# Kernel optimization log

Measured on AMD Instinct MI355X. Metric: run time of the kernel, lower is better.

Reference implementation:

```python
import jax, jax.numpy as jnp
import numpy as np

NUM_NODES = 94
SEQ_LEN = 784
OUT_CLASSES = 10
ALPHA = 0.5
GAMMA = 0.1
OMEGA = 2.0 * np.pi / 28.0
H = 1.0
INV_SQRT_N = 1.0 / np.sqrt(NUM_NODES)


def _xavier(key, shape):
    fan_in, fan_out = shape[1], shape[0]
    limit = np.sqrt(6.0 / (fan_in + fan_out))
    return jax.random.uniform(key, shape, jnp.float32, -limit, limit)


def setup_inputs() -> dict:
    key = jax.random.key(0)
    k_in, k_ih, k_hh, k_ro = jax.random.split(key, 4)
    batch = 1024
    return {
        "input_sequence": jax.random.normal(k_in, (batch, SEQ_LEN), jnp.float32),
        "w_ih": _xavier(k_ih, (NUM_NODES, 1)),   # Linear(1 -> N) weight
        "b_ih": jnp.zeros((NUM_NODES,), jnp.float32),
        "w_hh": _xavier(k_hh, (NUM_NODES, NUM_NODES)),  # Linear(N -> N) weight
        "b_hh": jnp.zeros((NUM_NODES,), jnp.float32),
        "w_ro": _xavier(k_ro, (OUT_CLASSES, NUM_NODES)),  # readout weight
        "b_ro": jnp.zeros((OUT_CLASSES,), jnp.float32),
    }


def reference(input_sequence, w_ih, b_ih, w_hh, b_hh, w_ro, b_ro):
    batch = input_sequence.shape[0]
    # precompute external drive for all steps: [T, B, N]
    # W_ih(s_t) with input_dim=1 is an outer product: s_t * w_ih[:,0] + b_ih
    s = input_sequence.T  # [T, B]
    w_ih_vec = w_ih[:, 0]  # [N]

    def step(carry, s_t):
        x, y = carry
        I_ext = s_t[:, None] * w_ih_vec[None, :] + b_ih  # [B, N]
        I_rec = y @ w_hh.T + b_hh                        # [B, N]
        A = (I_ext + I_rec) * INV_SQRT_N
        accel = ALPHA * jnp.tanh(A) - 2.0 * GAMMA * y - (OMEGA ** 2) * x
        x_new = x + H * y
        y_new = y + H * accel
        return (x_new, y_new), None

    x0 = jnp.zeros((batch, NUM_NODES), jnp.float32)
    y0 = jnp.zeros((batch, NUM_NODES), jnp.float32)
    (x_final, _), _ = jax.lax.scan(step, (x0, y0), s)
    return x_final @ w_ro.T + b_ro  # [B, 10]
```

## Files before the change

### kernel.cpp

```cpp
#include <hip/hip_runtime.h>
#include <math.h>

#define NUM_NODES 94
#define SEQ_LEN 784
#define OUT_CLASSES 10
#define EPB 16
#define NW 6
#define YP 104
#define SP 796

#define TWO_GAMMA 0.2f
#define OM2 0.0503551324598949f
#define INV_SQRT_N 0.103142124625879
#define LOG2E 1.4426950408889634
#define WSCALE ((float)(2.0 * INV_SQRT_N * LOG2E))

typedef _Float16 half8 __attribute__((ext_vector_type(8)));
typedef _Float16 half4 __attribute__((ext_vector_type(4)));
typedef float    floatx4 __attribute__((ext_vector_type(4)));
typedef float    f2 __attribute__((ext_vector_type(2)));

__global__
__attribute__((amdgpu_flat_work_group_size(NW*64, NW*64)))
void horn_kernel(
    const float* __restrict__ input,
    const float* __restrict__ w_ih,
    const float* __restrict__ b_ih,
    const float* __restrict__ w_hh,
    const float* __restrict__ b_hh,
    const float* __restrict__ w_ro,
    const float* __restrict__ b_ro,
    float* __restrict__ out)
{
    __shared__ __align__(16) float    sinl[EPB * SP];
    __shared__ __align__(16) _Float16 ybuf[2][EPB * YP];

    const int tid  = threadIdx.x;
    const int m    = tid >> 6;
    const int lane = tid & 63;
    const int e    = lane & 15;
    const int h    = lane >> 4;
    const int bb   = blockIdx.x;

    {
        const floatx4* in4 = (const floatx4*)(input + (size_t)bb * EPB * SEQ_LEN);
        for (int idx = tid; idx < EPB * (SEQ_LEN / 4); idx += NW * 64) {
            int ee = idx / (SEQ_LEN / 4);
            int cc = idx - ee * (SEQ_LEN / 4);
            *(floatx4*)&sinl[ee * SP + 4 * cc] = in4[idx];
        }
    }
    {
        float* yz = (float*)&ybuf[0][0];
        for (int i = tid; i < (2 * EPB * YP) / 2; i += NW * 64) yz[i] = 0.0f;
    }

    const int arow = 16 * m + e;
    half8 a0, a1, a2;
    #pragma unroll
    for (int i = 0; i < 8; i++) {
        const int kb = 8 * h + i;
        a0[i] = (_Float16)((arow < NUM_NODES && kb      < NUM_NODES) ? w_hh[arow * NUM_NODES + kb     ] * WSCALE : 0.0f);
        a1[i] = (_Float16)((arow < NUM_NODES && kb + 32 < NUM_NODES) ? w_hh[arow * NUM_NODES + kb + 32] * WSCALE : 0.0f);
        a2[i] = (_Float16)((arow < NUM_NODES && kb + 64 < NUM_NODES) ? w_hh[arow * NUM_NODES + kb + 64] * WSCALE : 0.0f);
    }

    const int r0 = 16 * m + 4 * h;
    f2 wih01, wih23, bias01, bias23;
    {
        float w[4], b[4];
        #pragma unroll
        for (int i = 0; i < 4; i++) {
            const int r = r0 + i;
            w[i] = (r < NUM_NODES) ? w_ih[r] * WSCALE : 0.0f;
            b[i] = (r < NUM_NODES) ? (b_ih[r] + b_hh[r]) * WSCALE : 0.0f;
        }
        wih01[0] = w[0]; wih01[1] = w[1]; wih23[0] = w[2]; wih23[1] = w[3];
        bias01[0] = b[0]; bias01[1] = b[1]; bias23[0] = b[2]; bias23[1] = b[3];
    }

    f2 x01 = {0.0f, 0.0f}, x23 = {0.0f, 0.0f};
    f2 y01 = {0.0f, 0.0f}, y23 = {0.0f, 0.0f};

    const int rdoff = e * YP + 8 * h;
    const int wroff = e * YP + r0;
    const int sbase = e * SP;

    const floatx4 zf4 = {0.0f, 0.0f, 0.0f, 0.0f};
    const f2 ng = {-TWO_GAMMA, -TWO_GAMMA};
    const f2 no = {-OM2, -OM2};

    __syncthreads();

    #define HSTEP(RD, WR, T) do {                                                  \
        half8 b0 = *(const half8*)&(RD)[rdoff];                                    \
        half8 b1 = *(const half8*)&(RD)[rdoff + 32];                               \
        half8 b2 = *(const half8*)&(RD)[rdoff + 64];                               \
        float st = sinl[sbase + (T)];                                              \
        floatx4 d0 = __builtin_amdgcn_mfma_f32_16x16x32_f16(a0, b0, zf4, 0, 0, 0); \
        floatx4 d1 = __builtin_amdgcn_mfma_f32_16x16x32_f16(a1, b1, zf4, 0, 0, 0); \
        floatx4 d2 = __builtin_amdgcn_mfma_f32_16x16x32_f16(a2, b2, zf4, 0, 0, 0); \
        f2 S01 = { d0[0] + d1[0] + d2[0], d0[1] + d1[1] + d2[1] };                 \
        f2 S23 = { d0[2] + d1[2] + d2[2], d0[3] + d1[3] + d2[3] };                 \
        f2 st2 = { st, st };                                                       \
        f2 e01 = st2 * wih01 + (bias01 + S01);                                     \
        f2 e23 = st2 * wih23 + (bias23 + S23);                                     \
        f2 t01, t23;                                                               \
        t01[0] = 0.5f - __builtin_amdgcn_rcpf(__builtin_amdgcn_exp2f(e01[0]) + 1.0f); \
        t01[1] = 0.5f - __builtin_amdgcn_rcpf(__builtin_amdgcn_exp2f(e01[1]) + 1.0f); \
        t23[0] = 0.5f - __builtin_amdgcn_rcpf(__builtin_amdgcn_exp2f(e23[0]) + 1.0f); \
        t23[1] = 0.5f - __builtin_amdgcn_rcpf(__builtin_amdgcn_exp2f(e23[1]) + 1.0f); \
        t01 = ng * y01 + t01;  t01 = no * x01 + t01;                               \
        t23 = ng * y23 + t23;  t23 = no * x23 + t23;                               \
        x01 += y01;  x23 += y23;                                                   \
        y01 += t01;  y23 += t23;                                                   \
        half4 yh;                                                                  \
        yh[0] = (_Float16)y01[0]; yh[1] = (_Float16)y01[1];                        \
        yh[2] = (_Float16)y23[0]; yh[3] = (_Float16)y23[1];                        \
        *(half4*)&(WR)[wroff] = yh;                                                \
        __syncthreads();                                                           \
    } while (0)

    for (int t = 0; t < SEQ_LEN; t += 2) {
        HSTEP(ybuf[0], ybuf[1], t);
        HSTEP(ybuf[1], ybuf[0], t + 1);
    }
    #undef HSTEP

    float* xsh = sinl;
    {
        floatx4 xv = { x01[0], x01[1], x23[0], x23[1] };
        *(floatx4*)&xsh[e * YP + r0] = xv;
    }
    __syncthreads();

    if (tid < EPB * OUT_CLASSES) {
        const int ee = tid / OUT_CLASSES;
        const int c  = tid - ee * OUT_CLASSES;
        float acc = b_ro[c];
        #pragma unroll 2
        for (int r = 0; r < NUM_NODES; r++)
            acc += xsh[ee * YP + r] * w_ro[c * NUM_NODES + r];
        out[((size_t)bb * EPB + ee) * OUT_CLASSES + c] = acc;
    }
}

extern "C" void kernel_launch(void* const* d_in, const int* in_sizes, int n_in,
                              void* d_out, int out_size, void* d_ws, size_t ws_size,
                              hipStream_t stream) {
    const float* input = (const float*)d_in[0];
    const float* w_ih  = (const float*)d_in[1];
    const float* b_ih  = (const float*)d_in[2];
    const float* w_hh  = (const float*)d_in[3];
    const float* b_hh  = (const float*)d_in[4];
    const float* w_ro  = (const float*)d_in[5];
    const float* b_ro  = (const float*)d_in[6];
    float* out = (float*)d_out;

    const int batch = in_sizes[0] / SEQ_LEN;
    dim3 grid(batch / EPB);
    dim3 block(NW * 64);

    hipLaunchKernelGGL(horn_kernel, grid, block, 0, stream,
                       input, w_ih, b_ih, w_hh, b_hh, w_ro, b_ro, out);
}
```

Before: 293.3 us.

## Process 32 batch elements per block with 4 waves each owning 48 rows

Doubles the batch elements per block to 32 and reorganizes work into 4 waves. Each wave handles 16 elements and 48 of the hidden rows, issuing 9 chained MFMAs per step with the bias folded into the accumulator. Because the larger element count no longer fits in LDS, input is staged in two halves of the sequence. The aim is fewer blocks and cheaper barriers among 4 waves instead of 6, at the cost of more serial MFMA and transcendental work per wave on each recurrent step and half as many blocks occupying CUs.

```diff
diff --git a/kernel.cpp b/kernel.cpp
--- a/kernel.cpp
+++ b/kernel.cpp
@@ -4,10 +4,10 @@
 #define NUM_NODES 94
 #define SEQ_LEN 784
 #define OUT_CLASSES 10
-#define EPB 16
-#define NW 6
+#define EPB 32
 #define YP 104
-#define SP 796
+#define SP 396
+#define THALF 392
 
 #define TWO_GAMMA 0.2f
 #define OM2 0.0503551324598949f
@@ -21,7 +21,7 @@
 typedef float    f2 __attribute__((ext_vector_type(2)));
 
 __global__
-__attribute__((amdgpu_flat_work_group_size(NW*64, NW*64)))
+__attribute__((amdgpu_flat_work_group_size(256, 256)))
 void horn_kernel(
     const float* __restrict__ input,
     const float* __restrict__ w_ih,
@@ -36,110 +36,127 @@
     __shared__ __align__(16) _Float16 ybuf[2][EPB * YP];
 
     const int tid  = threadIdx.x;
-    const int m    = tid >> 6;
+    const int w    = tid >> 6;
     const int lane = tid & 63;
+    const int g    = w >> 1;
+    const int tau  = w & 1;
     const int e    = lane & 15;
     const int h    = lane >> 4;
     const int bb   = blockIdx.x;
+    const int Eloc = 16 * g + e;
+    const int RB   = 48 * tau;
 
-    {
-        const floatx4* in4 = (const floatx4*)(input + (size_t)bb * EPB * SEQ_LEN);
-        for (int idx = tid; idx < EPB * (SEQ_LEN / 4); idx += NW * 64) {
-            int ee = idx / (SEQ_LEN / 4);
-            int cc = idx - ee * (SEQ_LEN / 4);
-            *(floatx4*)&sinl[ee * SP + 4 * cc] = in4[idx];
+    for (int i = tid; i < (2 * EPB * YP) / 2; i += 256) ((float*)ybuf)[i] = 0.0f;
+
+    half8 a[3][3];
+    floatx4 biasC[3];
+    f2 wih01[3], wih23[3];
+    #pragma unroll
+    for (int t3 = 0; t3 < 3; ++t3) {
+        const int arow = RB + 16 * t3 + e;
+        #pragma unroll
+        for (int c = 0; c < 3; ++c) {
+            #pragma unroll
+            for (int i = 0; i < 8; ++i) {
+                const int k = 32 * c + 8 * h + i;
+                a[t3][c][i] = (_Float16)((arow < NUM_NODES && k < NUM_NODES)
+                                ? w_hh[arow * NUM_NODES + k] * WSCALE : 0.0f);
+            }
         }
-    }
-    {
-        float* yz = (float*)&ybuf[0][0];
-        for (int i = tid; i < (2 * EPB * YP) / 2; i += NW * 64) yz[i] = 0.0f;
+        float bv[4], wv[4];
+        #pragma unroll
+        for (int r = 0; r < 4; ++r) {
+            const int R = RB + 16 * t3 + 4 * h + r;
+            bv[r] = (R < NUM_NODES) ? (b_ih[R] + b_hh[R]) * WSCALE : 0.0f;
+            wv[r] = (R < NUM_NODES) ? w_ih[R] * WSCALE : 0.0f;
+        }
+        biasC[t3][0] = bv[0]; biasC[t3][1] = bv[1]; biasC[t3][2] = bv[2]; biasC[t3][3] = bv[3];
+        wih01[t3][0] = wv[0]; wih01[t3][1] = wv[1];
+        wih23[t3][0] = wv[2]; wih23[t3][1] = wv[3];
     }
 
-    const int arow = 16 * m + e;
-    half8 a0, a1, a2;
+    f2 x01[3], x23[3], y01[3], y23[3];
     #pragma unroll
-    for (int i = 0; i < 8; i++) {
-        const int kb = 8 * h + i;
-        a0[i] = (_Float16)((arow < NUM_NODES && kb      < NUM_NODES) ? w_hh[arow * NUM_NODES + kb     ] * WSCALE : 0.0f);
-        a1[i] = (_Float16)((arow < NUM_NODES && kb + 32 < NUM_NODES) ? w_hh[arow * NUM_NODES + kb + 32] * WSCALE : 0.0f);
-        a2[i] = (_Float16)((arow < NUM_NODES && kb + 64 < NUM_NODES) ? w_hh[arow * NUM_NODES + kb + 64] * WSCALE : 0.0f);
+    for (int t3 = 0; t3 < 3; ++t3) {
+        x01[t3] = (f2){0.0f, 0.0f}; x23[t3] = (f2){0.0f, 0.0f};
+        y01[t3] = (f2){0.0f, 0.0f}; y23[t3] = (f2){0.0f, 0.0f};
     }
 
-    const int r0 = 16 * m + 4 * h;
-    f2 wih01, wih23, bias01, bias23;
-    {
-        float w[4], b[4];
-        #pragma unroll
-        for (int i = 0; i < 4; i++) {
-            const int r = r0 + i;
-            w[i] = (r < NUM_NODES) ? w_ih[r] * WSCALE : 0.0f;
-            b[i] = (r < NUM_NODES) ? (b_ih[r] + b_hh[r]) * WSCALE : 0.0f;
-        }
-        wih01[0] = w[0]; wih01[1] = w[1]; wih23[0] = w[2]; wih23[1] = w[3];
-        bias01[0] = b[0]; bias01[1] = b[1]; bias23[0] = b[2]; bias23[1] = b[3];
-    }
+    const int rb  = Eloc * YP + 8 * h;
+    const int wb0 = Eloc * YP + RB + 4 * h;
+    const int sb  = Eloc * SP;
 
-    f2 x01 = {0.0f, 0.0f}, x23 = {0.0f, 0.0f};
-    f2 y01 = {0.0f, 0.0f}, y23 = {0.0f, 0.0f};
-
-    const int rdoff = e * YP + 8 * h;
-    const int wroff = e * YP + r0;
-    const int sbase = e * SP;
-
-    const floatx4 zf4 = {0.0f, 0.0f, 0.0f, 0.0f};
     const f2 ng = {-TWO_GAMMA, -TWO_GAMMA};
     const f2 no = {-OM2, -OM2};
 
-    __syncthreads();
-
-    #define HSTEP(RD, WR, T) do {                                                  \
-        half8 b0 = *(const half8*)&(RD)[rdoff];                                    \
-        half8 b1 = *(const half8*)&(RD)[rdoff + 32];                               \
-        half8 b2 = *(const half8*)&(RD)[rdoff + 64];                               \
-        float st = sinl[sbase + (T)];                                              \
-        floatx4 d0 = __builtin_amdgcn_mfma_f32_16x16x32_f16(a0, b0, zf4, 0, 0, 0); \
-        floatx4 d1 = __builtin_amdgcn_mfma_f32_16x16x32_f16(a1, b1, zf4, 0, 0, 0); \
-        floatx4 d2 = __builtin_amdgcn_mfma_f32_16x16x32_f16(a2, b2, zf4, 0, 0, 0); \
-        f2 S01 = { d0[0] + d1[0] + d2[0], d0[1] + d1[1] + d2[1] };                 \
-        f2 S23 = { d0[2] + d1[2] + d2[2], d0[3] + d1[3] + d2[3] };                 \
-        f2 st2 = { st, st };                                                       \
-        f2 e01 = st2 * wih01 + (bias01 + S01);                                     \
-        f2 e23 = st2 * wih23 + (bias23 + S23);                                     \
-        f2 t01, t23;                                                               \
-        t01[0] = 0.5f - __builtin_amdgcn_rcpf(__builtin_amdgcn_exp2f(e01[0]) + 1.0f); \
-        t01[1] = 0.5f - __builtin_amdgcn_rcpf(__builtin_amdgcn_exp2f(e01[1]) + 1.0f); \
-        t23[0] = 0.5f - __builtin_amdgcn_rcpf(__builtin_amdgcn_exp2f(e23[0]) + 1.0f); \
-        t23[1] = 0.5f - __builtin_amdgcn_rcpf(__builtin_amdgcn_exp2f(e23[1]) + 1.0f); \
-        t01 = ng * y01 + t01;  t01 = no * x01 + t01;                               \
-        t23 = ng * y23 + t23;  t23 = no * x23 + t23;                               \
-        x01 += y01;  x23 += y23;                                                   \
-        y01 += t01;  y23 += t23;                                                   \
-        half4 yh;                                                                  \
-        yh[0] = (_Float16)y01[0]; yh[1] = (_Float16)y01[1];                        \
-        yh[2] = (_Float16)y23[0]; yh[3] = (_Float16)y23[1];                        \
-        *(half4*)&(WR)[wroff] = yh;                                                \
-        __syncthreads();                                                           \
+    #define HSTEP(RD, WR, T) do {                                                      \
+        const _Float16* yr = &(RD)[rb];                                                \
+        half8 B0 = *(const half8*)(yr);                                                \
+        half8 B1 = *(const half8*)(yr + 32);                                           \
+        half8 B2 = *(const half8*)(yr + 64);                                           \
+        float st = sinl[sb + (T)];                                                     \
+        f2 st2 = {st, st};                                                             \
+        _Float16* yw = &(WR)[wb0];                                                     \
+        _Pragma("unroll")                                                              \
+        for (int t3 = 0; t3 < 3; ++t3) {                                               \
+            floatx4 d = biasC[t3];                                                     \
+            d = __builtin_amdgcn_mfma_f32_16x16x32_f16(a[t3][0], B0, d, 0, 0, 0);      \
+            d = __builtin_amdgcn_mfma_f32_16x16x32_f16(a[t3][1], B1, d, 0, 0, 0);      \
+            d = __builtin_amdgcn_mfma_f32_16x16x32_f16(a[t3][2], B2, d, 0, 0, 0);      \
+            f2 S01 = {d[0], d[1]}, S23 = {d[2], d[3]};                                 \
+            f2 e01 = st2 * wih01[t3] + S01;                                            \
+            f2 e23 = st2 * wih23[t3] + S23;                                            \
+            f2 t01, t23;                                                               \
+            t01[0] = 0.5f - __builtin_amdgcn_rcpf(__builtin_amdgcn_exp2f(e01[0]) + 1.0f); \
+            t01[1] = 0.5f - __builtin_amdgcn_rcpf(__builtin_amdgcn_exp2f(e01[1]) + 1.0f); \
+            t23[0] = 0.5f - __builtin_amdgcn_rcpf(__builtin_amdgcn_exp2f(e23[0]) + 1.0f); \
+            t23[1] = 0.5f - __builtin_amdgcn_rcpf(__builtin_amdgcn_exp2f(e23[1]) + 1.0f); \
+            t01 = ng * y01[t3] + t01;  t01 = no * x01[t3] + t01;                       \
+            t23 = ng * y23[t3] + t23;  t23 = no * x23[t3] + t23;                       \
+            x01[t3] += y01[t3];  x23[t3] += y23[t3];                                   \
+            y01[t3] += t01;      y23[t3] += t23;                                       \
+            half4 yh;                                                                  \
+            yh[0] = (_Float16)y01[t3][0]; yh[1] = (_Float16)y01[t3][1];                \
+            yh[2] = (_Float16)y23[t3][0]; yh[3] = (_Float16)y23[t3][1];                \
+            *(half4*)(yw + 16 * t3) = yh;                                              \
+        }                                                                              \
+        __syncthreads();                                                               \
     } while (0)
 
-    for (int t = 0; t < SEQ_LEN; t += 2) {
-        HSTEP(ybuf[0], ybuf[1], t);
-        HSTEP(ybuf[1], ybuf[0], t + 1);
+    for (int hf = 0; hf < 2; ++hf) {
+        __syncthreads();
+        {
+            const float* src = input + (size_t)bb * EPB * SEQ_LEN + hf * THALF;
+            for (int idx = tid; idx < EPB * (THALF / 4); idx += 256) {
+                int ee = idx / (THALF / 4);
+                int cc = idx - ee * (THALF / 4);
+                *(floatx4*)&sinl[ee * SP + 4 * cc] =
+                    *(const floatx4*)(src + (size_t)ee * SEQ_LEN + 4 * cc);
+            }
+        }
+        __syncthreads();
+        for (int t = 0; t < THALF; t += 2) {
+            HSTEP(ybuf[0], ybuf[1], t);
+            HSTEP(ybuf[1], ybuf[0], t + 1);
+        }
     }
     #undef HSTEP
 
     float* xsh = sinl;
-    {
-        floatx4 xv = { x01[0], x01[1], x23[0], x23[1] };
-        *(floatx4*)&xsh[e * YP + r0] = xv;
+    #pragma unroll
+    for (int t3 = 0; t3 < 3; ++t3) {
+        floatx4 xv;
+        xv[0] = x01[t3][0]; xv[1] = x01[t3][1]; xv[2] = x23[t3][0]; xv[3] = x23[t3][1];
+        *(floatx4*)&xsh[Eloc * YP + RB + 16 * t3 + 4 * h] = xv;
     }
     __syncthreads();
 
-    if (tid < EPB * OUT_CLASSES) {
-        const int ee = tid / OUT_CLASSES;
-        const int c  = tid - ee * OUT_CLASSES;
+    for (int idx = tid; idx < EPB * OUT_CLASSES; idx += 256) {
+        const int ee = idx / OUT_CLASSES;
+        const int c  = idx - ee * OUT_CLASSES;
         float acc = b_ro[c];
         #pragma unroll 2
-        for (int r = 0; r < NUM_NODES; r++)
+        for (int r = 0; r < NUM_NODES; ++r)
             acc += xsh[ee * YP + r] * w_ro[c * NUM_NODES + r];
         out[((size_t)bb * EPB + ee) * OUT_CLASSES + c] = acc;
     }
@@ -159,7 +176,7 @@
 
     const int batch = in_sizes[0] / SEQ_LEN;
     dim3 grid(batch / EPB);
-    dim3 block(NW * 64);
+    dim3 block(256);
 
     hipLaunchKernelGGL(horn_kernel, grid, block, 0, stream,
                        input, w_ih, b_ih, w_hh, b_hh, w_ro, b_ro, out);
```

Result: slower. 405.0 us (+38.1%).

## Use four waves with uneven row-tile split and MFMA bias accumulation

Applied to the files above, without the earlier changes.

Reduces the workgroup from six waves to four. The first two waves each compute two 16-row tiles of the recurrent matvec and the last two waves compute one each. The bias is folded into the MFMA accumulator init and two of the three MFMAs are chained, which removes some adds. The next step's input sample is prefetched one step ahead to take its shared load off the critical path. Fewer waves means cheaper barriers, but it makes the work per step uneven, so waves 0 and 1 now sit on the per-step critical path with twice the MFMA and tanh work.

```diff
diff --git a/kernel.cpp b/kernel.cpp
--- a/kernel.cpp
+++ b/kernel.cpp
@@ -5,9 +5,9 @@
 #define SEQ_LEN 784
 #define OUT_CLASSES 10
 #define EPB 16
-#define NW 6
+#define NW 4
 #define YP 104
-#define SP 796
+#define SP 788
 
 #define TWO_GAMMA 0.2f
 #define OM2 0.0503551324598949f
@@ -36,88 +36,114 @@
     __shared__ __align__(16) _Float16 ybuf[2][EPB * YP];
 
     const int tid  = threadIdx.x;
-    const int m    = tid >> 6;
+    const int w    = tid >> 6;
     const int lane = tid & 63;
     const int e    = lane & 15;
     const int h    = lane >> 4;
     const int bb   = blockIdx.x;
+
+    const int  TA  = (w < 2) ? 2 * w : (w + 2);
+    const int  TB  = 2 * w + 1;
+    const bool two = (w < 2);
 
     {
         const floatx4* in4 = (const floatx4*)(input + (size_t)bb * EPB * SEQ_LEN);
         for (int idx = tid; idx < EPB * (SEQ_LEN / 4); idx += NW * 64) {
             int ee = idx / (SEQ_LEN / 4);
             int cc = idx - ee * (SEQ_LEN / 4);
-            *(floatx4*)&sinl[ee * SP + 4 * cc] = in4[idx];
+            *(floatx4*)&sinl[ee * SP + 4 * cc] = in4[ee * (SEQ_LEN / 4) + cc];
         }
     }
-    {
-        float* yz = (float*)&ybuf[0][0];
-        for (int i = tid; i < (2 * EPB * YP) / 2; i += NW * 64) yz[i] = 0.0f;
-    }
+    for (int i = tid; i < (2 * EPB * YP) / 2; i += NW * 64) ((float*)ybuf)[i] = 0.0f;
 
-    const int arow = 16 * m + e;
-    half8 a0, a1, a2;
-    #pragma unroll
-    for (int i = 0; i < 8; i++) {
-        const int kb = 8 * h + i;
-        a0[i] = (_Float16)((arow < NUM_NODES && kb      < NUM_NODES) ? w_hh[arow * NUM_NODES + kb     ] * WSCALE : 0.0f);
-        a1[i] = (_Float16)((arow < NUM_NODES && kb + 32 < NUM_NODES) ? w_hh[arow * NUM_NODES + kb + 32] * WSCALE : 0.0f);
-        a2[i] = (_Float16)((arow < NUM_NODES && kb + 64 < NUM_NODES) ? w_hh[arow * NUM_NODES + kb + 64] * WSCALE : 0.0f);
-    }
+    #define LOAD_TILE(T, A0, A1, A2, BIASC, WIH01, WIH23) do {                     \
+        const int arow = 16 * (T) + e;                                             \
+        _Pragma("unroll")                                                          \
+        for (int i = 0; i < 8; ++i) {                                              \
+            const int k = 8 * h + i;                                               \
+            (A0)[i] = (_Float16)((arow < NUM_NODES && k      < NUM_NODES)          \
+                        ? w_hh[arow * NUM_NODES + k     ] * WSCALE : 0.0f);        \
+            (A1)[i] = (_Float16)((arow < NUM_NODES && k + 32 < NUM_NODES)          \
+                        ? w_hh[arow * NUM_NODES + k + 32] * WSCALE : 0.0f);        \
+            (A2)[i] = (_Float16)((arow < NUM_NODES && k + 64 < NUM_NODES)          \
+                        ? w_hh[arow * NUM_NODES + k + 64] * WSCALE : 0.0f);        \
+        }                                                                          \
+        _Pragma("unroll")                                                          \
+        for (int r = 0; r < 4; ++r) {                                              \
+            const int R = 16 * (T) + 4 * h + r;                                    \
+            const float bv = (R < NUM_NODES) ? (b_ih[R] + b_hh[R]) * WSCALE : 0.0f;\
+            const float wv = (R < NUM_NODES) ? w_ih[R] * WSCALE : 0.0f;            \
+            (BIASC)[r] = bv;                                                       \
+            if (r < 2) (WIH01)[r] = wv; else (WIH23)[r - 2] = wv;                   \
+        }                                                                          \
+    } while (0)
 
-    const int r0 = 16 * m + 4 * h;
-    f2 wih01, wih23, bias01, bias23;
-    {
-        float w[4], b[4];
-        #pragma unroll
-        for (int i = 0; i < 4; i++) {
-            const int r = r0 + i;
-            w[i] = (r < NUM_NODES) ? w_ih[r] * WSCALE : 0.0f;
-            b[i] = (r < NUM_NODES) ? (b_ih[r] + b_hh[r]) * WSCALE : 0.0f;
-        }
-        wih01[0] = w[0]; wih01[1] = w[1]; wih23[0] = w[2]; wih23[1] = w[3];
-        bias01[0] = b[0]; bias01[1] = b[1]; bias23[0] = b[2]; bias23[1] = b[3];
-    }
+    half8 aA0, aA1, aA2, aB0, aB1, aB2;
+    floatx4 biasA = {0,0,0,0}, biasB = {0,0,0,0};
+    f2 wihA01 = {0,0}, wihA23 = {0,0}, wihB01 = {0,0}, wihB23 = {0,0};
+    LOAD_TILE(TA, aA0, aA1, aA2, biasA, wihA01, wihA23);
+    if (two) { LOAD_TILE(TB, aB0, aB1, aB2, biasB, wihB01, wihB23); }
+    #undef LOAD_TILE
 
-    f2 x01 = {0.0f, 0.0f}, x23 = {0.0f, 0.0f};
-    f2 y01 = {0.0f, 0.0f}, y23 = {0.0f, 0.0f};
+    f2 xA01 = {0,0}, xA23 = {0,0}, yA01 = {0,0}, yA23 = {0,0};
+    f2 xB01 = {0,0}, xB23 = {0,0}, yB01 = {0,0}, yB23 = {0,0};
 
-    const int rdoff = e * YP + 8 * h;
-    const int wroff = e * YP + r0;
-    const int sbase = e * SP;
+    const int rb  = e * YP + 8 * h;
+    const int wbA = e * YP + 16 * TA + 4 * h;
+    const int wbB = e * YP + 16 * TB + 4 * h;
+    const int sb  = e * SP;
 
-    const floatx4 zf4 = {0.0f, 0.0f, 0.0f, 0.0f};
+    const floatx4 zf4 = {0,0,0,0};
     const f2 ng = {-TWO_GAMMA, -TWO_GAMMA};
     const f2 no = {-OM2, -OM2};
 
     __syncthreads();
 
-    #define HSTEP(RD, WR, T) do {                                                  \
-        half8 b0 = *(const half8*)&(RD)[rdoff];                                    \
-        half8 b1 = *(const half8*)&(RD)[rdoff + 32];                               \
-        half8 b2 = *(const half8*)&(RD)[rdoff + 64];                               \
-        float st = sinl[sbase + (T)];                                              \
-        floatx4 d0 = __builtin_amdgcn_mfma_f32_16x16x32_f16(a0, b0, zf4, 0, 0, 0); \
-        floatx4 d1 = __builtin_amdgcn_mfma_f32_16x16x32_f16(a1, b1, zf4, 0, 0, 0); \
-        floatx4 d2 = __builtin_amdgcn_mfma_f32_16x16x32_f16(a2, b2, zf4, 0, 0, 0); \
-        f2 S01 = { d0[0] + d1[0] + d2[0], d0[1] + d1[1] + d2[1] };                 \
-        f2 S23 = { d0[2] + d1[2] + d2[2], d0[3] + d1[3] + d2[3] };                 \
+    float st = sinl[sb];
+
+    #define DYN(d, WIH01, WIH23, X01, X23, Y01, Y23, WR, WOFF) do {                \
         f2 st2 = { st, st };                                                       \
-        f2 e01 = st2 * wih01 + (bias01 + S01);                                     \
-        f2 e23 = st2 * wih23 + (bias23 + S23);                                     \
+        f2 e01 = st2 * (WIH01) + (f2){ (d)[0], (d)[1] };                           \
+        f2 e23 = st2 * (WIH23) + (f2){ (d)[2], (d)[3] };                           \
         f2 t01, t23;                                                               \
         t01[0] = 0.5f - __builtin_amdgcn_rcpf(__builtin_amdgcn_exp2f(e01[0]) + 1.0f); \
         t01[1] = 0.5f - __builtin_amdgcn_rcpf(__builtin_amdgcn_exp2f(e01[1]) + 1.0f); \
         t23[0] = 0.5f - __builtin_amdgcn_rcpf(__builtin_amdgcn_exp2f(e23[0]) + 1.0f); \
         t23[1] = 0.5f - __builtin_amdgcn_rcpf(__builtin_amdgcn_exp2f(e23[1]) + 1.0f); \
-        t01 = ng * y01 + t01;  t01 = no * x01 + t01;                               \
-        t23 = ng * y23 + t23;  t23 = no * x23 + t23;                               \
-        x01 += y01;  x23 += y23;                                                   \
-        y01 += t01;  y23 += t23;                                                   \
+        t01 = ng * (Y01) + t01;  t01 = no * (X01) + t01;                           \
+        t23 = ng * (Y23) + t23;  t23 = no * (X23) + t23;                           \
+        (X01) += (Y01);  (X23) += (Y23);                                           \
+        (Y01) += t01;    (Y23) += t23;                                             \
         half4 yh;                                                                  \
-        yh[0] = (_Float16)y01[0]; yh[1] = (_Float16)y01[1];                        \
-        yh[2] = (_Float16)y23[0]; yh[3] = (_Float16)y23[1];                        \
-        *(half4*)&(WR)[wroff] = yh;                                                \
+        yh[0] = (_Float16)(Y01)[0]; yh[1] = (_Float16)(Y01)[1];                    \
+        yh[2] = (_Float16)(Y23)[0]; yh[3] = (_Float16)(Y23)[1];                    \
+        *(half4*)&(WR)[WOFF] = yh;                                                 \
+    } while (0)
+
+    #define HSTEP(RD, WR, T) do {                                                  \
+        const _Float16* yr = &(RD)[rb];                                            \
+        half8 B0 = *(const half8*)(yr);                                            \
+        half8 B1 = *(const half8*)(yr + 32);                                       \
+        half8 B2 = *(const half8*)(yr + 64);                                       \
+        const int tn = ((T) + 1 < SEQ_LEN) ? (T) + 1 : (SEQ_LEN - 1);              \
+        float stn = sinl[sb + tn];                                                 \
+                         \
+        floatx4 dA  = __builtin_amdgcn_mfma_f32_16x16x32_f16(aA0, B0, biasA, 0, 0, 0); \
+        floatx4 dA2 = __builtin_amdgcn_mfma_f32_16x16x32_f16(aA1, B1, zf4,  0, 0, 0); \
+        dA = __builtin_amdgcn_mfma_f32_16x16x32_f16(aA2, B2, dA, 0, 0, 0);         \
+        if (two) {                                                                 \
+            floatx4 dB  = __builtin_amdgcn_mfma_f32_16x16x32_f16(aB0, B0, biasB, 0, 0, 0); \
+            floatx4 dB2 = __builtin_amdgcn_mfma_f32_16x16x32_f16(aB1, B1, zf4,  0, 0, 0); \
+            dB = __builtin_amdgcn_mfma_f32_16x16x32_f16(aB2, B2, dB, 0, 0, 0);     \
+            dB += dB2;                                                             \
+            dA += dA2;                                                             \
+            DYN(dA, wihA01, wihA23, xA01, xA23, yA01, yA23, WR, wbA);              \
+            DYN(dB, wihB01, wihB23, xB01, xB23, yB01, yB23, WR, wbB);              \
+        } else {                                                                   \
+            dA += dA2;                                                             \
+            DYN(dA, wihA01, wihA23, xA01, xA23, yA01, yA23, WR, wbA);              \
+        }                                                                          \
+        st = stn;                                                                  \
         __syncthreads();                                                           \
     } while (0)
 
@@ -126,20 +152,27 @@
         HSTEP(ybuf[1], ybuf[0], t + 1);
     }
     #undef HSTEP
+    #undef DYN
 
     float* xsh = sinl;
     {
-        floatx4 xv = { x01[0], x01[1], x23[0], x23[1] };
-        *(floatx4*)&xsh[e * YP + r0] = xv;
+        floatx4 xv;
+        xv[0] = xA01[0]; xv[1] = xA01[1]; xv[2] = xA23[0]; xv[3] = xA23[1];
+        *(floatx4*)&xsh[e * YP + 16 * TA + 4 * h] = xv;
+        if (two) {
+            floatx4 xw;
+            xw[0] = xB01[0]; xw[1] = xB01[1]; xw[2] = xB23[0]; xw[3] = xB23[1];
+            *(floatx4*)&xsh[e * YP + 16 * TB + 4 * h] = xw;
+        }
     }
     __syncthreads();
 
-    if (tid < EPB * OUT_CLASSES) {
-        const int ee = tid / OUT_CLASSES;
-        const int c  = tid - ee * OUT_CLASSES;
+    for (int idx = tid; idx < EPB * OUT_CLASSES; idx += NW * 64) {
+        const int ee = idx / OUT_CLASSES;
+        const int c  = idx - ee * OUT_CLASSES;
         float acc = b_ro[c];
         #pragma unroll 2
-        for (int r = 0; r < NUM_NODES; r++)
+        for (int r = 0; r < NUM_NODES; ++r)
             acc += xsh[ee * YP + r] * w_ro[c * NUM_NODES + r];
         out[((size_t)bb * EPB + ee) * OUT_CLASSES + c] = acc;
     }
```

New measurement: 332.8 us. +13.4%, slower.

## Fold input drive and bias into MFMA via augmented y columns

Applied to the files above, without the earlier changes.

Folds the external drive and bias into the recurrent matrix product. The A matrix gains two extra columns (w_ih and the combined bias), and the y buffer carries the next input sample and a constant 1 in columns 94 and 95, written each step by one duty lane group. The y row stride gets an e-dependent pad to change the LDS bank mapping, and the damping/spring update is regrouped so that only a subtraction follows the tanh. This removes per-lane input loads and FMAs from the critical path, at the cost of rounding the input and bias to fp16, extra divergent branches, and a tail-store special case.

```diff
diff --git a/kernel.cpp b/kernel.cpp
--- a/kernel.cpp
+++ b/kernel.cpp
@@ -6,8 +6,8 @@
 #define OUT_CLASSES 10
 #define EPB 16
 #define NW 6
-#define YP 104
-#define SP 796
+#define SP 788
+#define YHALF 1664
 
 #define TWO_GAMMA 0.2f
 #define OM2 0.0503551324598949f
@@ -17,6 +17,7 @@
 
 typedef _Float16 half8 __attribute__((ext_vector_type(8)));
 typedef _Float16 half4 __attribute__((ext_vector_type(4)));
+typedef _Float16 half2v __attribute__((ext_vector_type(2)));
 typedef float    floatx4 __attribute__((ext_vector_type(4)));
 typedef float    f2 __attribute__((ext_vector_type(2)));
 
@@ -33,104 +34,124 @@
     float* __restrict__ out)
 {
     __shared__ __align__(16) float    sinl[EPB * SP];
-    __shared__ __align__(16) _Float16 ybuf[2][EPB * YP];
+    __shared__ __align__(16) _Float16 ybuf[2][YHALF];
 
     const int tid  = threadIdx.x;
-    const int m    = tid >> 6;
+    const int w    = tid >> 6;
     const int lane = tid & 63;
     const int e    = lane & 15;
     const int h    = lane >> 4;
     const int bb   = blockIdx.x;
+
+    const int  T        = w;
+    const bool duty     = (w == 3 && h == 0);
+    const bool tailmask = (w == 5 && h == 3);
+
+    const int eoff = 104 * e + 4 * (e >> 3);
 
     {
         const floatx4* in4 = (const floatx4*)(input + (size_t)bb * EPB * SEQ_LEN);
         for (int idx = tid; idx < EPB * (SEQ_LEN / 4); idx += NW * 64) {
             int ee = idx / (SEQ_LEN / 4);
             int cc = idx - ee * (SEQ_LEN / 4);
-            *(floatx4*)&sinl[ee * SP + 4 * cc] = in4[idx];
+            *(floatx4*)&sinl[ee * SP + 4 * cc] = in4[ee * (SEQ_LEN / 4) + cc];
         }
     }
-    {
-        float* yz = (float*)&ybuf[0][0];
-        for (int i = tid; i < (2 * EPB * YP) / 2; i += NW * 64) yz[i] = 0.0f;
+    for (int i = tid; i < (2 * YHALF) / 2; i += NW * 64) ((float*)ybuf)[i] = 0.0f;
+
+    const int arow = 16 * T + e;
+    half8 a0, a1, a2;
+    #pragma unroll
+    for (int i = 0; i < 8; ++i) {
+        const int k = 8 * h + i;
+        float v0 = 0.0f, v1 = 0.0f, v2 = 0.0f;
+        if (arow < NUM_NODES) {
+            v0 = w_hh[arow * NUM_NODES + k] * WSCALE;
+            if (k + 32 < NUM_NODES) v1 = w_hh[arow * NUM_NODES + k + 32] * WSCALE;
+            const int k2 = k + 64;
+            if      (k2 <  NUM_NODES) v2 = w_hh[arow * NUM_NODES + k2] * WSCALE;
+            else if (k2 == NUM_NODES) v2 = w_ih[arow] * WSCALE;
+            else                      v2 = (b_ih[arow] + b_hh[arow]) * WSCALE;
+        }
+        a0[i] = (_Float16)v0; a1[i] = (_Float16)v1; a2[i] = (_Float16)v2;
     }
 
-    const int arow = 16 * m + e;
-    half8 a0, a1, a2;
-    #pragma unroll
-    for (int i = 0; i < 8; i++) {
-        const int kb = 8 * h + i;
-        a0[i] = (_Float16)((arow < NUM_NODES && kb      < NUM_NODES) ? w_hh[arow * NUM_NODES + kb     ] * WSCALE : 0.0f);
-        a1[i] = (_Float16)((arow < NUM_NODES && kb + 32 < NUM_NODES) ? w_hh[arow * NUM_NODES + kb + 32] * WSCALE : 0.0f);
-        a2[i] = (_Float16)((arow < NUM_NODES && kb + 64 < NUM_NODES) ? w_hh[arow * NUM_NODES + kb + 64] * WSCALE : 0.0f);
-    }
+    f2 x01 = {0,0}, x23 = {0,0}, y01 = {0,0}, y23 = {0,0};
 
-    const int r0 = 16 * m + 4 * h;
-    f2 wih01, wih23, bias01, bias23;
-    {
-        float w[4], b[4];
-        #pragma unroll
-        for (int i = 0; i < 4; i++) {
-            const int r = r0 + i;
-            w[i] = (r < NUM_NODES) ? w_ih[r] * WSCALE : 0.0f;
-            b[i] = (r < NUM_NODES) ? (b_ih[r] + b_hh[r]) * WSCALE : 0.0f;
-        }
-        wih01[0] = w[0]; wih01[1] = w[1]; wih23[0] = w[2]; wih23[1] = w[3];
-        bias01[0] = b[0]; bias01[1] = b[1]; bias23[0] = b[2]; bias23[1] = b[3];
-    }
-
-    f2 x01 = {0.0f, 0.0f}, x23 = {0.0f, 0.0f};
-    f2 y01 = {0.0f, 0.0f}, y23 = {0.0f, 0.0f};
-
-    const int rdoff = e * YP + 8 * h;
-    const int wroff = e * YP + r0;
-    const int sbase = e * SP;
-
-    const floatx4 zf4 = {0.0f, 0.0f, 0.0f, 0.0f};
-    const f2 ng = {-TWO_GAMMA, -TWO_GAMMA};
-    const f2 no = {-OM2, -OM2};
+    const floatx4 zf4 = {0,0,0,0};
+    const f2 no2 = {-OM2, -OM2};
+    const f2 p82 = {1.0f - TWO_GAMMA, 1.0f - TWO_GAMMA};
+    const f2 h05 = {0.5f, 0.5f};
 
     __syncthreads();
 
-    #define HSTEP(RD, WR, T) do {                                                  \
-        half8 b0 = *(const half8*)&(RD)[rdoff];                                    \
-        half8 b1 = *(const half8*)&(RD)[rdoff + 32];                               \
-        half8 b2 = *(const half8*)&(RD)[rdoff + 64];                               \
-        float st = sinl[sbase + (T)];                                              \
-        floatx4 d0 = __builtin_amdgcn_mfma_f32_16x16x32_f16(a0, b0, zf4, 0, 0, 0); \
-        floatx4 d1 = __builtin_amdgcn_mfma_f32_16x16x32_f16(a1, b1, zf4, 0, 0, 0); \
-        floatx4 d2 = __builtin_amdgcn_mfma_f32_16x16x32_f16(a2, b2, zf4, 0, 0, 0); \
-        f2 S01 = { d0[0] + d1[0] + d2[0], d0[1] + d1[1] + d2[1] };                 \
-        f2 S23 = { d0[2] + d1[2] + d2[2], d0[3] + d1[3] + d2[3] };                 \
-        f2 st2 = { st, st };                                                       \
-        f2 e01 = st2 * wih01 + (bias01 + S01);                                     \
-        f2 e23 = st2 * wih23 + (bias23 + S23);                                     \
-        f2 t01, t23;                                                               \
-        t01[0] = 0.5f - __builtin_amdgcn_rcpf(__builtin_amdgcn_exp2f(e01[0]) + 1.0f); \
-        t01[1] = 0.5f - __builtin_amdgcn_rcpf(__builtin_amdgcn_exp2f(e01[1]) + 1.0f); \
-        t23[0] = 0.5f - __builtin_amdgcn_rcpf(__builtin_amdgcn_exp2f(e23[0]) + 1.0f); \
-        t23[1] = 0.5f - __builtin_amdgcn_rcpf(__builtin_amdgcn_exp2f(e23[1]) + 1.0f); \
-        t01 = ng * y01 + t01;  t01 = no * x01 + t01;                               \
-        t23 = ng * y23 + t23;  t23 = no * x23 + t23;                               \
+    if (tid < EPB) {
+        const int eo = 104 * tid + 4 * (tid >> 3);
+        const float s0 = input[((size_t)bb * EPB + tid) * SEQ_LEN];
+        half2v v0; v0[0] = (_Float16)s0; v0[1] = (_Float16)1.0f;
+        half2v v1; v1[0] = (_Float16)0.0f; v1[1] = (_Float16)1.0f;
+        *(half2v*)&ybuf[0][eo + NUM_NODES] = v0;
+        *(half2v*)&ybuf[1][eo + NUM_NODES] = v1;
+    }
+    __syncthreads();
+
+    #define HSTEP(RP, WP, T_) do {                                                 \
+        const _Float16* Yb = &ybuf[RP][eoff + 8 * h];                              \
+        half4 l0 = *(const half4*)(Yb);                                            \
+        half4 u0 = *(const half4*)(Yb + 4);                                        \
+        half4 l1 = *(const half4*)(Yb + 32);                                       \
+        half4 u1 = *(const half4*)(Yb + 36);                                       \
+        half4 l2 = *(const half4*)(Yb + 64);                                       \
+        half4 u2 = *(const half4*)(Yb + 68);                                       \
+                                \
+        f2 q01 = no2 * x01 + h05;  q01 = p82 * y01 + q01;                          \
+        f2 q23 = no2 * x23 + h05;  q23 = p82 * y23 + q23;                          \
         x01 += y01;  x23 += y23;                                                   \
-        y01 += t01;  y23 += t23;                                                   \
+        float snext = 0.0f;                                                        \
+        if (duty) {                                                                \
+            const int tn = ((T_) + 1 < SEQ_LEN) ? (T_) + 1 : (SEQ_LEN - 1);        \
+            snext = sinl[e * SP + tn];                                             \
+        }                                                                          \
+        half8 B0 = __builtin_shufflevector(l0, u0, 0, 1, 2, 3, 4, 5, 6, 7);        \
+        half8 B1 = __builtin_shufflevector(l1, u1, 0, 1, 2, 3, 4, 5, 6, 7);        \
+        half8 B2 = __builtin_shufflevector(l2, u2, 0, 1, 2, 3, 4, 5, 6, 7);        \
+        floatx4 d0 = __builtin_amdgcn_mfma_f32_16x16x32_f16(a0, B0, zf4, 0, 0, 0); \
+        floatx4 d1 = __builtin_amdgcn_mfma_f32_16x16x32_f16(a1, B1, zf4, 0, 0, 0); \
+        floatx4 d2 = __builtin_amdgcn_mfma_f32_16x16x32_f16(a2, B2, zf4, 0, 0, 0); \
+        floatx4 d = (d0 + d1) + d2;    \
+        f2 r01, r23;                                                               \
+        r01[0] = __builtin_amdgcn_rcpf(__builtin_amdgcn_exp2f(d[0]) + 1.0f);       \
+        r01[1] = __builtin_amdgcn_rcpf(__builtin_amdgcn_exp2f(d[1]) + 1.0f);       \
+        r23[0] = __builtin_amdgcn_rcpf(__builtin_amdgcn_exp2f(d[2]) + 1.0f);       \
+        r23[1] = __builtin_amdgcn_rcpf(__builtin_amdgcn_exp2f(d[3]) + 1.0f);       \
+        y01 = q01 - r01;  y23 = q23 - r23;                                         \
         half4 yh;                                                                  \
         yh[0] = (_Float16)y01[0]; yh[1] = (_Float16)y01[1];                        \
         yh[2] = (_Float16)y23[0]; yh[3] = (_Float16)y23[1];                        \
-        *(half4*)&(WR)[wroff] = yh;                                                \
+        if (tailmask) {                                                            \
+            half2v yt; yt[0] = yh[0]; yt[1] = yh[1];          \
+            *(half2v*)&ybuf[WP][eoff + 92] = yt;                                   \
+        } else {                                                                   \
+            *(half4*)&ybuf[WP][eoff + 16 * T + 4 * h] = yh;                        \
+        }                                                                          \
+        if (duty) {                                                                \
+            half2v sv; sv[0] = (_Float16)snext; sv[1] = (_Float16)1.0f;            \
+            *(half2v*)&ybuf[WP][eoff + NUM_NODES] = sv;                            \
+        }                                                                          \
         __syncthreads();                                                           \
     } while (0)
 
     for (int t = 0; t < SEQ_LEN; t += 2) {
-        HSTEP(ybuf[0], ybuf[1], t);
-        HSTEP(ybuf[1], ybuf[0], t + 1);
+        HSTEP(0, 1, t);
+        HSTEP(1, 0, t + 1);
     }
     #undef HSTEP
 
     float* xsh = sinl;
     {
-        floatx4 xv = { x01[0], x01[1], x23[0], x23[1] };
-        *(floatx4*)&xsh[e * YP + r0] = xv;
+        floatx4 xv;
+        xv[0] = x01[0]; xv[1] = x01[1]; xv[2] = x23[0]; xv[3] = x23[1];
+        *(floatx4*)&xsh[e * 104 + 16 * T + 4 * h] = xv;
     }
     __syncthreads();
 
@@ -139,8 +160,8 @@
         const int c  = tid - ee * OUT_CLASSES;
         float acc = b_ro[c];
         #pragma unroll 2
-        for (int r = 0; r < NUM_NODES; r++)
-            acc += xsh[ee * YP + r] * w_ro[c * NUM_NODES + r];
+        for (int r = 0; r < NUM_NODES; ++r)
+            acc += xsh[ee * 104 + r] * w_ro[c * NUM_NODES + r];
         out[((size_t)bb * EPB + ee) * OUT_CLASSES + c] = acc;
     }
 }
```

Result: slower. 303.4 us (+3.4%).
